# Performance work log

Hardware: AMD Instinct MI355X
Metric: run time of the kernel (lower is better)

The kernel has to match this reference:

```python
import jax, jax.numpy as jnp
import numpy as np
from jax import lax

DN = ('NCHW', 'OIHW', 'NCHW')
BN_EPS = 1e-5


def _conv(x, w, pad):
    # pad: list of (lo, hi) for H, W
    return lax.conv_general_dilated(x, w, (1, 1), pad, dimension_numbers=DN)


def _grid_sample_bilinear(img, grid):
    """F.grid_sample(img, grid, align_corners=True, padding_mode='zeros').
    img: [N,C,H,W], grid: [N,Ho,Wo,2] with (x,y) in [-1,1]."""
    N, C, H, W = img.shape
    gx, gy = grid[..., 0], grid[..., 1]
    # align_corners=True mapping to pixel coords
    ix = (gx + 1.0) * 0.5 * (W - 1)
    iy = (gy + 1.0) * 0.5 * (H - 1)
    x0 = jnp.floor(ix)
    y0 = jnp.floor(iy)
    x1 = x0 + 1.0
    y1 = y0 + 1.0
    # bilinear weights
    wa = (x1 - ix) * (y1 - iy)  # top-left (x0,y0)
    wb = (ix - x0) * (y1 - iy)  # top-right (x1,y0)
    wc = (x1 - ix) * (iy - y0)  # bottom-left (x0,y1)
    wd = (ix - x0) * (iy - y0)  # bottom-right (x1,y1)

    imgc = jnp.transpose(img, (0, 2, 3, 1))  # [N,H,W,C]
    b = jnp.arange(N)[:, None, None]

    def gather(xi, yi):
        valid = (xi >= 0) & (xi <= W - 1) & (yi >= 0) & (yi <= H - 1)
        xc = jnp.clip(xi, 0, W - 1).astype(jnp.int32)
        yc = jnp.clip(yi, 0, H - 1).astype(jnp.int32)
        v = imgc[b, yc, xc]  # [N,Ho,Wo,C]
        return v * valid[..., None].astype(img.dtype)

    out = (gather(x0, y0) * wa[..., None] + gather(x1, y0) * wb[..., None]
           + gather(x0, y1) * wc[..., None] + gather(x1, y1) * wd[..., None])
    return jnp.transpose(out, (0, 3, 1, 2))  # [N,C,Ho,Wo]


def setup_inputs() -> dict:
    key = jax.random.key(0)
    ks = jax.random.split(key, 12)
    N, C1, C2 = 8, 512, 256
    H, W = 64, 64
    x1 = jax.random.normal(ks[0], (N, C1, 2 * H, 2 * W), dtype=jnp.float32)
    x2 = jax.random.normal(ks[1], (N, C2, H, W), dtype=jnp.float32)
    w_change = jax.random.normal(ks[2], (C2, C1, 1, 1), dtype=jnp.float32) * 0.02
    b_change = jax.random.normal(ks[3], (C2,), dtype=jnp.float32) * 0.02
    w_cc1 = jax.random.normal(ks[4], (C2, 2 * C2, 1, 1), dtype=jnp.float32) * 0.02
    bn_gamma = 1.0 + 0.1 * jax.random.normal(ks[5], (C2,), dtype=jnp.float32)
    bn_beta = 0.1 * jax.random.normal(ks[6], (C2,), dtype=jnp.float32)
    bn_mean = 0.1 * jax.random.normal(ks[7], (C2,), dtype=jnp.float32)
    bn_var = jax.random.uniform(ks[8], (C2,), dtype=jnp.float32, minval=0.5, maxval=1.5)
    w_cc2 = jax.random.normal(ks[9], (4, C2, 3, 3), dtype=jnp.float32) * 0.02
    return {"x1": x1, "x2": x2, "w_change": w_change, "b_change": b_change,
            "w_cc1": w_cc1, "bn_gamma": bn_gamma, "bn_beta": bn_beta,
            "bn_mean": bn_mean, "bn_var": bn_var, "w_cc2": w_cc2}


def reference(x1, x2, w_change, b_change, w_cc1, bn_gamma, bn_beta, bn_mean, bn_var, w_cc2):
    # MaxPool2d(2,2)
    x1p = lax.reduce_window(x1, -jnp.inf, lax.max, (1, 1, 2, 2), (1, 1, 2, 2), 'VALID')
    # change: 1x1 conv with bias
    x1c = _conv(x1p, w_change, [(0, 0), (0, 0)]) + b_change[None, :, None, None]
    # concat + concat_conv (1x1 conv -> BN(eval) -> ReLU -> 3x3 conv)
    x = jnp.concatenate([x1c, x2], axis=1)
    x = _conv(x, w_cc1, [(0, 0), (0, 0)])
    inv = lax.rsqrt(bn_var + BN_EPS)
    x = (x - bn_mean[None, :, None, None]) * (inv * bn_gamma)[None, :, None, None] + bn_beta[None, :, None, None]
    x = jax.nn.relu(x)
    flow = _conv(x, w_cc2, [(1, 1), (1, 1)])  # [N,4,H,W]
    flow1 = flow[:, :2]
    flow2 = flow[:, 2:]

    N, _, H, W = x1c.shape
    # base grid: [...,0]=x over width, [...,1]=y over height
    xs = jnp.linspace(-1.0, 1.0, W, dtype=x1c.dtype)
    ys = jnp.linspace(-1.0, 1.0, H, dtype=x1c.dtype)
    base = jnp.stack(jnp.meshgrid(xs, ys, indexing='xy'), axis=-1)  # [H,W,2]
    norm = jnp.array([(W - 1) / 2.0, (H - 1) / 2.0], dtype=x1c.dtype)

    grid1 = base[None] + jnp.transpose(flow1, (0, 2, 3, 1)) / norm
    grid2 = base[None] + jnp.transpose(flow2, (0, 2, 3, 1)) / norm

    u1 = _grid_sample_bilinear(x1c, grid1)
    u2 = _grid_sample_bilinear(x2, grid2)
    return u1 + u2
```

## Files before the change

### kernel.cpp

```cpp
#include <hip/hip_runtime.h>
#include <hip/hip_bf16.h>

#define NB 8
#define C1 512
#define C2 256
#define HWSZ 4096
#define BN_EPS 1e-5f
#define P2 264

typedef __hip_bfloat16 bf16;
typedef __hip_bfloat162 bf162;
typedef __attribute__((ext_vector_type(8))) short short8v;
typedef __attribute__((ext_vector_type(4))) float f32x4;

static __device__ inline float b2f(bf16 h) { return __bfloat162float(h); }

static __device__ inline float us2f(unsigned short u) {
  union { unsigned u32; float f; } c; c.u32 = ((unsigned)u) << 16; return c.f;
}

static __device__ inline unsigned short f2bf(float f) {
  union { bf16 h; unsigned short u; } c;
  c.h = __float2bfloat16(f);
  return c.u;
}

static __device__ inline unsigned pack2(float a, float b) {
  union { unsigned u; bf162 h; } pk;
  pk.h = __float22bfloat162_rn(make_float2(a, b));
  return pk.u;
}

static __device__ inline uint2 pack4(float a, float b, float c, float d) {
  union { uint2 u; bf162 h[2]; } pk;
  pk.h[0] = __float22bfloat162_rn(make_float2(a, b));
  pk.h[1] = __float22bfloat162_rn(make_float2(c, d));
  return pk.u;
}

#define SBARQ() asm volatile("s_waitcnt lgkmcnt(0)\n\ts_barrier" ::: "memory")
#define SBAR()  asm volatile("s_barrier" ::: "memory")
#define LGKM0() asm volatile("s_waitcnt lgkmcnt(0)" ::: "memory")

__global__ __launch_bounds__(256) void k0_swizzle(
    const float* __restrict__ wch, const float* __restrict__ wcc1,
    unsigned short* __restrict__ wchB, unsigned short* __restrict__ wcc1B) {
  const int t = blockIdx.x * 256 + threadIdx.x;
  const int which = t >> 17;
  const int r = t & 131071;
  const int i = r & 7;
  const int lane = (r >> 3) & 63;
  const int ntile = (r >> 9) & 15;
  const int kstep = r >> 13;
  const int ci = kstep * 32 + (lane >> 4) * 8 + i;
  const int co = ntile * 16 + (lane & 15);
  const float* s = which ? wcc1 : wch;
  unsigned short* d = which ? wcc1B : wchB;
  d[r] = f2bf(s[co * 512 + ci]);
}

__global__ __launch_bounds__(512) void k12_fused(
    const float* __restrict__ x1, const float* __restrict__ x2,
    const unsigned short* __restrict__ wchB, const unsigned short* __restrict__ wcc1B,
    const float* __restrict__ bch,
    const float* __restrict__ gamma, const float* __restrict__ beta,
    const float* __restrict__ mean, const float* __restrict__ var,
    unsigned short* __restrict__ x1c_nhwc, unsigned short* __restrict__ x2_nhwc,
    bf16* __restrict__ xbn) {
  __shared__ unsigned short As[64 * 40];
  __shared__ unsigned short As2[64 * P2];
  const int tid = threadIdx.x;
  const int lane = tid & 63;
  const int wv = tid >> 6;
  const int lrow = lane & 15;
  const int lgrp = lane >> 4;

  const int m0g = blockIdx.x * 64;
  const int n = m0g >> 12;
  const int hw0 = m0g & 4095;
  const int h = hw0 >> 6;

  f32x4 acc[4][2];
#pragma unroll
  for (int mt = 0; mt < 4; ++mt)
#pragma unroll
    for (int nt = 0; nt < 2; ++nt) acc[mt][nt] = (f32x4){0.f, 0.f, 0.f, 0.f};

  const int pmi = tid & 31;
  const int ms = pmi * 2;
  const int ch0 = (tid >> 5) * 2;

  const float* x1p = x1 + (size_t)n * C1 * 16384 + (size_t)(2 * h) * 128 + 2 * ms;

  float4 t0, b0, t1, b1;
#define LOADA(K0_) do { \
    const float* p_ = x1p + (size_t)((K0_) + ch0) * 16384; \
    t0 = *(const float4*)p_;            b0 = *(const float4*)(p_ + 128); \
    t1 = *(const float4*)(p_ + 16384);  b1 = *(const float4*)(p_ + 16384 + 128); \
  } while (0)
#define POOLA(U0_, U1_) do { \
    U0_ = pack2(fmaxf(fmaxf(t0.x, t0.y), fmaxf(b0.x, b0.y)), \
                fmaxf(fmaxf(t1.x, t1.y), fmaxf(b1.x, b1.y))); \
    U1_ = pack2(fmaxf(fmaxf(t0.z, t0.w), fmaxf(b0.z, b0.w)), \
                fmaxf(fmaxf(t1.z, t1.w), fmaxf(b1.z, b1.w))); \
  } while (0)

  unsigned uA0, uA1;
  LOADA(0);
  POOLA(uA0, uA1);
  LOADA(32);

  for (int ks = 0; ks < 16; ++ks) {
    SBARQ();
    *(unsigned*)&As[ms * 40 + ch0] = uA0;
    *(unsigned*)&As[(ms + 1) * 40 + ch0] = uA1;
    LGKM0();
    SBAR();

    unsigned uN0, uN1;
    if (ks < 15) {
      POOLA(uN0, uN1);
      if (ks < 14) LOADA((ks + 2) * 32);
    }

    short8v a[4];
#pragma unroll
    for (int mt = 0; mt < 4; ++mt)
      a[mt] = *(const short8v*)&As[(mt * 16 + lrow) * 40 + lgrp * 8];
#pragma unroll
    for (int nt = 0; nt < 2; ++nt) {
      const int ntile = wv * 2 + nt;
      const short8v b = *(const short8v*)&wchB[(size_t)((ks * 16 + ntile) * 64 + lane) * 8];
#pragma unroll
      for (int mt = 0; mt < 4; ++mt)
        acc[mt][nt] = __builtin_amdgcn_mfma_f32_16x16x32_bf16(a[mt], b, acc[mt][nt], 0, 0, 0);
    }
    if (ks < 15) { uA0 = uN0; uA1 = uN1; }
  }

  const int chB = tid >> 4;
  const int mqB = (tid & 15) * 4;
  float4 cf0 = *(const float4*)&x2[((size_t)(n * C2 + chB)) * HWSZ + hw0 + mqB];
  float4 cf1 = *(const float4*)&x2[((size_t)(n * C2 + 32 + chB)) * HWSZ + hw0 + mqB];

#pragma unroll
  for (int nt = 0; nt < 2; ++nt) {
    const int co = (wv * 2 + nt) * 16 + lrow;
    const float bias = bch[co];
#pragma unroll
    for (int mt = 0; mt < 4; ++mt) {
      const f32x4 v = acc[mt][nt];
      const uint2 pk = pack4(v.x + bias, v.y + bias, v.z + bias, v.w + bias);
      const int mb = mt * 16 + lgrp * 4;
      As2[(mb + 0) * P2 + co] = (unsigned short)(pk.x & 0xffffu);
      As2[(mb + 1) * P2 + co] = (unsigned short)(pk.x >> 16);
      As2[(mb + 2) * P2 + co] = (unsigned short)(pk.y & 0xffffu);
      As2[(mb + 3) * P2 + co] = (unsigned short)(pk.y >> 16);
      acc[mt][nt] = (f32x4){0.f, 0.f, 0.f, 0.f};
    }
  }
  LGKM0();
  SBAR();

  {
    const int mm = tid >> 3;
    const int cg = (tid & 7) * 32;
    const size_t ob = ((size_t)(m0g + mm)) * 256 + cg;
#pragma unroll
    for (int k = 0; k < 4; ++k) {
      const uint4 v = *(const uint4*)&As2[mm * P2 + cg + k * 8];
      *(uint4*)&x1c_nhwc[ob + k * 8] = v;
    }
  }

#pragma unroll
  for (int ks = 0; ks < 8; ++ks) {
    short8v a[4];
#pragma unroll
    for (int mt = 0; mt < 4; ++mt)
      a[mt] = *(const short8v*)&As2[(mt * 16 + lrow) * P2 + ks * 32 + lgrp * 8];
#pragma unroll
    for (int nt = 0; nt < 2; ++nt) {
      const int ntile = wv * 2 + nt;
      const short8v b = *(const short8v*)&wcc1B[(size_t)((ks * 16 + ntile) * 64 + lane) * 8];
#pragma unroll
      for (int mt = 0; mt < 4; ++mt)
        acc[mt][nt] = __builtin_amdgcn_mfma_f32_16x16x32_bf16(a[mt], b, acc[mt][nt], 0, 0, 0);
    }
  }

  for (int ks = 8; ks < 16; ++ks) {
    const unsigned p0 = pack2(cf0.x, cf0.y);
    const unsigned p1 = pack2(cf0.z, cf0.w);
    cf0 = cf1;
    if (ks < 14) {
      cf1 = *(const float4*)&x2[((size_t)(n * C2 + (ks - 6) * 32 + chB)) * HWSZ + hw0 + mqB];
    }
    SBARQ();
    As[(mqB + 0) * 40 + chB] = (unsigned short)(p0 & 0xffffu);
    As[(mqB + 1) * 40 + chB] = (unsigned short)(p0 >> 16);
    As[(mqB + 2) * 40 + chB] = (unsigned short)(p1 & 0xffffu);
    As[(mqB + 3) * 40 + chB] = (unsigned short)(p1 >> 16);
    LGKM0();
    SBAR();

    {
      const int m = tid >> 3;
      const int c4 = (tid & 7) * 4;
      const uint2 v = *(const uint2*)&As[m * 40 + c4];
      *(uint2*)&x2_nhwc[((size_t)(m0g + m)) * 256 + (ks - 8) * 32 + c4] = v;
    }

    short8v a[4];
#pragma unroll
    for (int mt = 0; mt < 4; ++mt)
      a[mt] = *(const short8v*)&As[(mt * 16 + lrow) * 40 + lgrp * 8];
#pragma unroll
    for (int nt = 0; nt < 2; ++nt) {
      const int ntile = wv * 2 + nt;
      const short8v b = *(const short8v*)&wcc1B[(size_t)((ks * 16 + ntile) * 64 + lane) * 8];
#pragma unroll
      for (int mt = 0; mt < 4; ++mt)
        acc[mt][nt] = __builtin_amdgcn_mfma_f32_16x16x32_bf16(a[mt], b, acc[mt][nt], 0, 0, 0);
    }
  }

#pragma unroll
  for (int nt = 0; nt < 2; ++nt) {
    const int co = (wv * 2 + nt) * 16 + lrow;
    const float sc = gamma[co] * rsqrtf(var[co] + BN_EPS);
    const float sh = beta[co] - mean[co] * sc;
#pragma unroll
    for (int mt = 0; mt < 4; ++mt) {
      const f32x4 vv = acc[mt][nt];
      *(uint2*)&xbn[((size_t)(n * C2 + co)) * HWSZ + hw0 + mt * 16 + lgrp * 4] =
          pack4(fmaxf(vv.x * sc + sh, 0.f), fmaxf(vv.y * sc + sh, 0.f),
                fmaxf(vv.z * sc + sh, 0.f), fmaxf(vv.w * sc + sh, 0.f));
    }
  }
#undef LOADA
#undef POOLA
}

__global__ __launch_bounds__(1024) void k34_conv_sample(
    const bf16* __restrict__ xbn, const float* __restrict__ wcc2,
    const unsigned short* __restrict__ x1c_nhwc,
    const unsigned short* __restrict__ x2_nhwc,
    float* __restrict__ out) {
  __shared__ float wsm[9216];
  __shared__ float part[16][4][64];
  __shared__ float flr[4][64];
  const int tid = threadIdx.x;
  const int n = blockIdx.x >> 6;
  const int h = blockIdx.x & 63;
  const int wl = tid & 63;
  const int q = tid >> 6;

  for (int idx = tid; idx < 9216; idx += 1024) {
    const int f = idx / 2304;
    const int r = idx % 2304;
    const int ci = r / 9;
    const int t = r % 9;
    wsm[ci * 36 + (t / 3) * 12 + (t % 3) * 4 + f] = wcc2[idx];
  }
  __syncthreads();

  float acc[4] = {0.f, 0.f, 0.f, 0.f};
  {
    const bf16* base = xbn + ((size_t)(n * C2 + q * 16)) * HWSZ;
    const float* wq = wsm + (q * 16) * 36;
    for (int cc = 0; cc < 16; ++cc) {
      const bf16* src = base + (size_t)cc * HWSZ;
      const float* wc = wq + cc * 36;
#pragma unroll
      for (int dy = 0; dy < 3; ++dy) {
        const int y = h + dy - 1;
        if ((unsigned)y >= 64u) continue;
        const float v = b2f(src[y * 64 + wl]);
        float vm = __shfl_up(v, 1);
        float vp = __shfl_down(v, 1);
        if (wl == 0) vm = 0.f;
        if (wl == 63) vp = 0.f;
        const float4 wa = *(const float4*)&wc[dy * 12 + 0];
        const float4 wb = *(const float4*)&wc[dy * 12 + 4];
        const float4 wd = *(const float4*)&wc[dy * 12 + 8];
        acc[0] = fmaf(vm, wa.x, fmaf(v, wb.x, fmaf(vp, wd.x, acc[0])));
        acc[1] = fmaf(vm, wa.y, fmaf(v, wb.y, fmaf(vp, wd.y, acc[1])));
        acc[2] = fmaf(vm, wa.z, fmaf(v, wb.z, fmaf(vp, wd.z, acc[2])));
        acc[3] = fmaf(vm, wa.w, fmaf(v, wb.w, fmaf(vp, wd.w, acc[3])));
      }
    }
  }
  part[q][0][wl] = acc[0];
  part[q][1][wl] = acc[1];
  part[q][2][wl] = acc[2];
  part[q][3][wl] = acc[3];
  __syncthreads();
  if (tid < 256) {
    const int f = tid >> 6;
    const int ww = tid & 63;
    float s = 0.f;
#pragma unroll
    for (int qq = 0; qq < 16; ++qq) s += part[qq][f][ww];
    flr[f][ww] = s;
  }
  __syncthreads();

  const float fx1 = flr[0][wl];
  const float fy1 = flr[1][wl];
  const float fx2 = flr[2][wl];
  const float fy2 = flr[3][wl];

  int oA1, oB1, oC1, oD1; float wa1, wb1, wc1, wd1;
  {
    const float ix = (float)wl + fx1, iy = (float)h + fy1;
    const float x0f = floorf(ix), y0f = floorf(iy);
    const float fx = ix - x0f, fy = iy - y0f;
    const int x0 = (int)x0f, y0 = (int)y0f, x1i = x0 + 1, y1i = y0 + 1;
    const float vx0 = (x0 >= 0 && x0 < 64) ? 1.f : 0.f;
    const float vx1 = (x1i >= 0 && x1i < 64) ? 1.f : 0.f;
    const float vy0 = (y0 >= 0 && y0 < 64) ? 1.f : 0.f;
    const float vy1 = (y1i >= 0 && y1i < 64) ? 1.f : 0.f;
    const int cx0 = min(max(x0, 0), 63), cx1 = min(max(x1i, 0), 63);
    const int cy0 = min(max(y0, 0), 63), cy1 = min(max(y1i, 0), 63);
    oA1 = cy0 * 64 + cx0; oB1 = cy0 * 64 + cx1;
    oC1 = cy1 * 64 + cx0; oD1 = cy1 * 64 + cx1;
    wa1 = (1.f - fx) * (1.f - fy) * vx0 * vy0;
    wb1 = fx * (1.f - fy) * vx1 * vy0;
    wc1 = (1.f - fx) * fy * vx0 * vy1;
    wd1 = fx * fy * vx1 * vy1;
  }
  int oA2, oB2, oC2, oD2; float wa2, wb2, wc2, wd2;
  {
    const float ix = (float)wl + fx2, iy = (float)h + fy2;
    const float x0f = floorf(ix), y0f = floorf(iy);
    const float fx = ix - x0f, fy = iy - y0f;
    const int x0 = (int)x0f, y0 = (int)y0f, x1i = x0 + 1, y1i = y0 + 1;
    const float vx0 = (x0 >= 0 && x0 < 64) ? 1.f : 0.f;
    const float vx1 = (x1i >= 0 && x1i < 64) ? 1.f : 0.f;
    const float vy0 = (y0 >= 0 && y0 < 64) ? 1.f : 0.f;
    const float vy1 = (y1i >= 0 && y1i < 64) ? 1.f : 0.f;
    const int cx0 = min(max(x0, 0), 63), cx1 = min(max(x1i, 0), 63);
    const int cy0 = min(max(y0, 0), 63), cy1 = min(max(y1i, 0), 63);
    oA2 = cy0 * 64 + cx0; oB2 = cy0 * 64 + cx1;
    oC2 = cy1 * 64 + cx0; oD2 = cy1 * 64 + cx1;
    wa2 = (1.f - fx) * (1.f - fy) * vx0 * vy0;
    wb2 = fx * (1.f - fy) * vx1 * vy0;
    wc2 = (1.f - fx) * fy * vx0 * vy1;
    wd2 = fx * fy * vx1 * vy1;
  }

  float u[16];
#pragma unroll
  for (int i = 0; i < 16; ++i) u[i] = 0.f;

  const unsigned short* p1 = x1c_nhwc + ((size_t)n * HWSZ) * 256 + q * 16;
  const unsigned short* p2 = x2_nhwc + ((size_t)n * HWSZ) * 256 + q * 16;

#define TAP(PB_, OFF_, WT_) do { \
    const unsigned short* tp_ = (PB_) + (size_t)(OFF_) * 256; \
    const uint4 v0_ = *(const uint4*)tp_; \
    const uint4 v1_ = *(const uint4*)(tp_ + 8); \
    const unsigned va_[8] = {v0_.x, v0_.y, v0_.z, v0_.w, v1_.x, v1_.y, v1_.z, v1_.w}; \
    _Pragma("unroll") \
    for (int k_ = 0; k_ < 8; ++k_) { \
      u[2 * k_ + 0] = fmaf((WT_), us2f((unsigned short)(va_[k_] & 0xffffu)), u[2 * k_ + 0]); \
      u[2 * k_ + 1] = fmaf((WT_), us2f((unsigned short)(va_[k_] >> 16)),    u[2 * k_ + 1]); \
    } \
  } while (0)

  TAP(p1, oA1, wa1); TAP(p1, oB1, wb1); TAP(p1, oC1, wc1); TAP(p1, oD1, wd1);
  TAP(p2, oA2, wa2); TAP(p2, oB2, wb2); TAP(p2, oC2, wc2); TAP(p2, oD2, wd2);
#undef TAP

  const size_t ob = ((size_t)(n * C2 + q * 16)) * HWSZ + h * 64 + wl;
#pragma unroll
  for (int i = 0; i < 16; ++i) out[ob + (size_t)i * HWSZ] = u[i];
}

extern "C" void kernel_launch(void* const* d_in, const int* in_sizes, int n_in,
                              void* d_out, int out_size, void* d_ws, size_t ws_size,
                              hipStream_t stream) {
  const float* x1      = (const float*)d_in[0];
  const float* x2      = (const float*)d_in[1];
  const float* w_change= (const float*)d_in[2];
  const float* b_change= (const float*)d_in[3];
  const float* w_cc1   = (const float*)d_in[4];
  const float* bn_gamma= (const float*)d_in[5];
  const float* bn_beta = (const float*)d_in[6];
  const float* bn_mean = (const float*)d_in[7];
  const float* bn_var  = (const float*)d_in[8];
  const float* w_cc2   = (const float*)d_in[9];
  float* out = (float*)d_out;

  unsigned short* x1c_nhwc = (unsigned short*)d_ws;
  bf16*           xbn      = (bf16*)((char*)d_ws + (16u << 20));
  unsigned short* x2_nhwc  = (unsigned short*)((char*)d_ws + (32u << 20));
  unsigned short* wchB     = (unsigned short*)((char*)d_ws + (48u << 20));
  unsigned short* wcc1B    = (unsigned short*)((char*)d_ws + (48u << 20) + (256u << 10));

  k0_swizzle<<<1024, 256, 0, stream>>>(w_change, w_cc1, wchB, wcc1B);
  k12_fused<<<512, 512, 0, stream>>>(x1, x2, wchB, wcc1B, b_change,
                                     bn_gamma, bn_beta, bn_mean, bn_var,
                                     x1c_nhwc, x2_nhwc, xbn);
  k34_conv_sample<<<512, 1024, 0, stream>>>(xbn, w_cc2, x1c_nhwc, x2_nhwc, out);
}
```

Measured before the change: 142.6 us.

## Precompute conv weight reorder and restructure grid-sample gather for coalescing

Moves the 3x3 conv weight reordering out of every k34 block into the one-time swizzle kernel, so each block now just copies pre-reordered weights into shared memory. The bilinear sampling is reorganized: 64 threads compute tap offsets and weights into shared memory, then each lane gathers 4 adjacent channels, so a wavefront reads contiguous channel segments of one pixel. Results are transposed through a shared buffer that reuses the weight storage, giving coalesced NCHW stores. This adds extra barriers and more, smaller gather loads in exchange for better coalescing.

```diff
diff --git a/kernel.cpp b/kernel.cpp
--- a/kernel.cpp
+++ b/kernel.cpp
@@ -44,19 +44,30 @@
 
 __global__ __launch_bounds__(256) void k0_swizzle(
     const float* __restrict__ wch, const float* __restrict__ wcc1,
-    unsigned short* __restrict__ wchB, unsigned short* __restrict__ wcc1B) {
+    const float* __restrict__ wcc2,
+    unsigned short* __restrict__ wchB, unsigned short* __restrict__ wcc1B,
+    float* __restrict__ wr) {
   const int t = blockIdx.x * 256 + threadIdx.x;
-  const int which = t >> 17;
-  const int r = t & 131071;
-  const int i = r & 7;
-  const int lane = (r >> 3) & 63;
-  const int ntile = (r >> 9) & 15;
-  const int kstep = r >> 13;
-  const int ci = kstep * 32 + (lane >> 4) * 8 + i;
-  const int co = ntile * 16 + (lane & 15);
-  const float* s = which ? wcc1 : wch;
-  unsigned short* d = which ? wcc1B : wchB;
-  d[r] = f2bf(s[co * 512 + ci]);
+  if (t < 262144) {
+    const int which = t >> 17;
+    const int r = t & 131071;
+    const int i = r & 7;
+    const int lane = (r >> 3) & 63;
+    const int ntile = (r >> 9) & 15;
+    const int kstep = r >> 13;
+    const int ci = kstep * 32 + (lane >> 4) * 8 + i;
+    const int co = ntile * 16 + (lane & 15);
+    const float* s = which ? wcc1 : wch;
+    unsigned short* d = which ? wcc1B : wchB;
+    d[r] = f2bf(s[co * 512 + ci]);
+  } else if (t < 262144 + 9216) {
+    const int r = t - 262144;
+    const int f = r / 2304;
+    const int rr = r % 2304;
+    const int ci = rr / 9;
+    const int tt = rr % 9;
+    wr[ci * 36 + (tt / 3) * 12 + (tt % 3) * 4 + f] = wcc2[r];
+  }
 }
 
 __global__ __launch_bounds__(512) void k12_fused(
@@ -243,32 +254,31 @@
 }
 
 __global__ __launch_bounds__(1024) void k34_conv_sample(
-    const bf16* __restrict__ xbn, const float* __restrict__ wcc2,
+    const bf16* __restrict__ xbn, const float* __restrict__ wr,
     const unsigned short* __restrict__ x1c_nhwc,
     const unsigned short* __restrict__ x2_nhwc,
     float* __restrict__ out) {
-  __shared__ float wsm[9216];
-  __shared__ float part[16][4][64];
+  __shared__ union {
+    struct { float wsm[9216]; float part[16][4][64]; } c;
+    float outT[256][65];
+  } sh;
   __shared__ float flr[4][64];
+  __shared__ int   toff[8][64];
+  __shared__ float twt[8][64];
+
   const int tid = threadIdx.x;
   const int n = blockIdx.x >> 6;
   const int h = blockIdx.x & 63;
   const int wl = tid & 63;
   const int q = tid >> 6;
 
-  for (int idx = tid; idx < 9216; idx += 1024) {
-    const int f = idx / 2304;
-    const int r = idx % 2304;
-    const int ci = r / 9;
-    const int t = r % 9;
-    wsm[ci * 36 + (t / 3) * 12 + (t % 3) * 4 + f] = wcc2[idx];
-  }
+  for (int idx = tid; idx < 9216; idx += 1024) sh.c.wsm[idx] = wr[idx];
   __syncthreads();
 
   float acc[4] = {0.f, 0.f, 0.f, 0.f};
   {
     const bf16* base = xbn + ((size_t)(n * C2 + q * 16)) * HWSZ;
-    const float* wq = wsm + (q * 16) * 36;
+    const float* wq = sh.c.wsm + (q * 16) * 36;
     for (int cc = 0; cc < 16; ++cc) {
       const bf16* src = base + (size_t)cc * HWSZ;
       const float* wc = wq + cc * 36;
@@ -291,91 +301,83 @@
       }
     }
   }
-  part[q][0][wl] = acc[0];
-  part[q][1][wl] = acc[1];
-  part[q][2][wl] = acc[2];
-  part[q][3][wl] = acc[3];
+  sh.c.part[q][0][wl] = acc[0];
+  sh.c.part[q][1][wl] = acc[1];
+  sh.c.part[q][2][wl] = acc[2];
+  sh.c.part[q][3][wl] = acc[3];
   __syncthreads();
   if (tid < 256) {
     const int f = tid >> 6;
     const int ww = tid & 63;
     float s = 0.f;
 #pragma unroll
-    for (int qq = 0; qq < 16; ++qq) s += part[qq][f][ww];
+    for (int qq = 0; qq < 16; ++qq) s += sh.c.part[qq][f][ww];
     flr[f][ww] = s;
   }
   __syncthreads();
 
-  const float fx1 = flr[0][wl];
-  const float fy1 = flr[1][wl];
-  const float fx2 = flr[2][wl];
-  const float fy2 = flr[3][wl];
-
-  int oA1, oB1, oC1, oD1; float wa1, wb1, wc1, wd1;
+  if (tid < 64) {
+    const float fxv[2] = {flr[0][tid], flr[2][tid]};
+    const float fyv[2] = {flr[1][tid], flr[3][tid]};
+#pragma unroll
+    for (int s = 0; s < 2; ++s) {
+      const float ix = (float)tid + fxv[s], iy = (float)h + fyv[s];
+      const float x0f = floorf(ix), y0f = floorf(iy);
+      const float fx = ix - x0f, fy = iy - y0f;
+      const int x0 = (int)x0f, y0 = (int)y0f, x1i = x0 + 1, y1i = y0 + 1;
+      const float vx0 = (x0 >= 0 && x0 < 64) ? 1.f : 0.f;
+      const float vx1 = (x1i >= 0 && x1i < 64) ? 1.f : 0.f;
+      const float vy0 = (y0 >= 0 && y0 < 64) ? 1.f : 0.f;
+      const float vy1 = (y1i >= 0 && y1i < 64) ? 1.f : 0.f;
+      const int cx0 = min(max(x0, 0), 63), cx1 = min(max(x1i, 0), 63);
+      const int cy0 = min(max(y0, 0), 63), cy1 = min(max(y1i, 0), 63);
+      toff[s * 4 + 0][tid] = cy0 * 64 + cx0;
+      toff[s * 4 + 1][tid] = cy0 * 64 + cx1;
+      toff[s * 4 + 2][tid] = cy1 * 64 + cx0;
+      toff[s * 4 + 3][tid] = cy1 * 64 + cx1;
+      twt[s * 4 + 0][tid] = (1.f - fx) * (1.f - fy) * vx0 * vy0;
+      twt[s * 4 + 1][tid] = fx * (1.f - fy) * vx1 * vy0;
+      twt[s * 4 + 2][tid] = (1.f - fx) * fy * vx0 * vy1;
+      twt[s * 4 + 3][tid] = fx * fy * vx1 * vy1;
+    }
+  }
+  __syncthreads();
+
   {
-    const float ix = (float)wl + fx1, iy = (float)h + fy1;
-    const float x0f = floorf(ix), y0f = floorf(iy);
-    const float fx = ix - x0f, fy = iy - y0f;
-    const int x0 = (int)x0f, y0 = (int)y0f, x1i = x0 + 1, y1i = y0 + 1;
-    const float vx0 = (x0 >= 0 && x0 < 64) ? 1.f : 0.f;
-    const float vx1 = (x1i >= 0 && x1i < 64) ? 1.f : 0.f;
-    const float vy0 = (y0 >= 0 && y0 < 64) ? 1.f : 0.f;
-    const float vy1 = (y1i >= 0 && y1i < 64) ? 1.f : 0.f;
-    const int cx0 = min(max(x0, 0), 63), cx1 = min(max(x1i, 0), 63);
-    const int cy0 = min(max(y0, 0), 63), cy1 = min(max(y1i, 0), 63);
-    oA1 = cy0 * 64 + cx0; oB1 = cy0 * 64 + cx1;
-    oC1 = cy1 * 64 + cx0; oD1 = cy1 * 64 + cx1;
-    wa1 = (1.f - fx) * (1.f - fy) * vx0 * vy0;
-    wb1 = fx * (1.f - fy) * vx1 * vy0;
-    wc1 = (1.f - fx) * fy * vx0 * vy1;
-    wd1 = fx * fy * vx1 * vy1;
-  }
-  int oA2, oB2, oC2, oD2; float wa2, wb2, wc2, wd2;
+    const unsigned short* pb1 = x1c_nhwc + (size_t)n * HWSZ * 256 + wl * 4;
+    const unsigned short* pb2 = x2_nhwc + (size_t)n * HWSZ * 256 + wl * 4;
+#pragma unroll
+    for (int pp = 0; pp < 4; ++pp) {
+      const int p = q * 4 + pp;
+      float u0 = 0.f, u1 = 0.f, u2 = 0.f, u3 = 0.f;
+#pragma unroll
+      for (int t = 0; t < 8; ++t) {
+        const int off = toff[t][p];
+        const float wt = twt[t][p];
+        const unsigned short* rp = (t < 4 ? pb1 : pb2) + (size_t)off * 256;
+        const uint2 v = *(const uint2*)rp;
+        u0 = fmaf(wt, us2f((unsigned short)(v.x & 0xffffu)), u0);
+        u1 = fmaf(wt, us2f((unsigned short)(v.x >> 16)), u1);
+        u2 = fmaf(wt, us2f((unsigned short)(v.y & 0xffffu)), u2);
+        u3 = fmaf(wt, us2f((unsigned short)(v.y >> 16)), u3);
+      }
+      sh.outT[wl * 4 + 0][p] = u0;
+      sh.outT[wl * 4 + 1][p] = u1;
+      sh.outT[wl * 4 + 2][p] = u2;
+      sh.outT[wl * 4 + 3][p] = u3;
+    }
+  }
+  __syncthreads();
+
   {
-    const float ix = (float)wl + fx2, iy = (float)h + fy2;
-    const float x0f = floorf(ix), y0f = floorf(iy);
-    const float fx = ix - x0f, fy = iy - y0f;
-    const int x0 = (int)x0f, y0 = (int)y0f, x1i = x0 + 1, y1i = y0 + 1;
-    const float vx0 = (x0 >= 0 && x0 < 64) ? 1.f : 0.f;
-    const float vx1 = (x1i >= 0 && x1i < 64) ? 1.f : 0.f;
-    const float vy0 = (y0 >= 0 && y0 < 64) ? 1.f : 0.f;
-    const float vy1 = (y1i >= 0 && y1i < 64) ? 1.f : 0.f;
-    const int cx0 = min(max(x0, 0), 63), cx1 = min(max(x1i, 0), 63);
-    const int cy0 = min(max(y0, 0), 63), cy1 = min(max(y1i, 0), 63);
-    oA2 = cy0 * 64 + cx0; oB2 = cy0 * 64 + cx1;
-    oC2 = cy1 * 64 + cx0; oD2 = cy1 * 64 + cx1;
-    wa2 = (1.f - fx) * (1.f - fy) * vx0 * vy0;
-    wb2 = fx * (1.f - fy) * vx1 * vy0;
-    wc2 = (1.f - fx) * fy * vx0 * vy1;
-    wd2 = fx * fy * vx1 * vy1;
-  }
-
-  float u[16];
-#pragma unroll
-  for (int i = 0; i < 16; ++i) u[i] = 0.f;
-
-  const unsigned short* p1 = x1c_nhwc + ((size_t)n * HWSZ) * 256 + q * 16;
-  const unsigned short* p2 = x2_nhwc + ((size_t)n * HWSZ) * 256 + q * 16;
-
-#define TAP(PB_, OFF_, WT_) do { \
-    const unsigned short* tp_ = (PB_) + (size_t)(OFF_) * 256; \
-    const uint4 v0_ = *(const uint4*)tp_; \
-    const uint4 v1_ = *(const uint4*)(tp_ + 8); \
-    const unsigned va_[8] = {v0_.x, v0_.y, v0_.z, v0_.w, v1_.x, v1_.y, v1_.z, v1_.w}; \
-    _Pragma("unroll") \
-    for (int k_ = 0; k_ < 8; ++k_) { \
-      u[2 * k_ + 0] = fmaf((WT_), us2f((unsigned short)(va_[k_] & 0xffffu)), u[2 * k_ + 0]); \
-      u[2 * k_ + 1] = fmaf((WT_), us2f((unsigned short)(va_[k_] >> 16)),    u[2 * k_ + 1]); \
-    } \
-  } while (0)
-
-  TAP(p1, oA1, wa1); TAP(p1, oB1, wb1); TAP(p1, oC1, wc1); TAP(p1, oD1, wd1);
-  TAP(p2, oA2, wa2); TAP(p2, oB2, wb2); TAP(p2, oC2, wc2); TAP(p2, oD2, wd2);
-#undef TAP
-
-  const size_t ob = ((size_t)(n * C2 + q * 16)) * HWSZ + h * 64 + wl;
-#pragma unroll
-  for (int i = 0; i < 16; ++i) out[ob + (size_t)i * HWSZ] = u[i];
+    const int p = tid & 63;
+    const int cg = (tid >> 6) * 16;
+    const size_t ob = ((size_t)(n * C2 + cg)) * HWSZ + h * 64 + p;
+#pragma unroll
+    for (int j = 0; j < 16; ++j) {
+      out[ob + (size_t)j * HWSZ] = sh.outT[cg + j][p];
+    }
+  }
 }
 
 extern "C" void kernel_launch(void* const* d_in, const int* in_sizes, int n_in,
@@ -398,10 +400,11 @@
   unsigned short* x2_nhwc  = (unsigned short*)((char*)d_ws + (32u << 20));
   unsigned short* wchB     = (unsigned short*)((char*)d_ws + (48u << 20));
   unsigned short* wcc1B    = (unsigned short*)((char*)d_ws + (48u << 20) + (256u << 10));
-
-  k0_swizzle<<<1024, 256, 0, stream>>>(w_change, w_cc1, wchB, wcc1B);
+  float*          wr       = (float*)((char*)d_ws + (48u << 20) + (512u << 10));
+
+  k0_swizzle<<<1060, 256, 0, stream>>>(w_change, w_cc1, w_cc2, wchB, wcc1B, wr);
   k12_fused<<<512, 512, 0, stream>>>(x1, x2, wchB, wcc1B, b_change,
                                      bn_gamma, bn_beta, bn_mean, bn_var,
                                      x1c_nhwc, x2_nhwc, xbn);
-  k34_conv_sample<<<512, 1024, 0, stream>>>(xbn, w_cc2, x1c_nhwc, x2_nhwc, out);
-}
+  k34_conv_sample<<<512, 1024, 0, stream>>>(xbn, wr, x1c_nhwc, x2_nhwc, out);
+}
```

Measured after the change: 139.5 us. -2.2%, faster.
